# Optimization experiments

Hardware: AMD Instinct MI355X
Metric: run time of the kernel (lower is better)

Reference implementation:

```python
import jax, jax.numpy as jnp
import numpy as np

N, E, G = 40000, 640000, 64
D, H, O = 128, 128, 10
EPS = 1e-5


def _lin(k, fan_in, shape):
    b = 1.0 / np.sqrt(fan_in)
    return jax.random.uniform(k, shape, jnp.float32, -b, b)


def setup_inputs() -> dict:
    key = jax.random.key(0)
    ks = jax.random.split(key, 12)
    x = jax.random.normal(ks[0], (N, D), jnp.float32)
    edge_index = jax.random.randint(ks[1], (2, E), 0, N)
    batch = jnp.sort(jax.random.randint(ks[2], (N,), 0, G))
    return {
        "x": x,
        "edge_index": edge_index,
        "batch": batch,
        "num_graphs": G,
        "W_gcn": _lin(ks[3], D, (D, H)),
        "b_gcn": jnp.zeros((H,), jnp.float32),
        "gamma": jnp.ones((H,), jnp.float32),
        "beta": jnp.zeros((H,), jnp.float32),
        "W1": _lin(ks[4], 3 * H, (3 * H, H)),
        "b1": _lin(ks[5], 3 * H, (H,)),
        "W2": _lin(ks[6], H, (H, H // 2)),
        "b2": _lin(ks[7], H, (H // 2,)),
        "W3": _lin(ks[8], H // 2, (H // 2, O)),
        "b3": _lin(ks[9], H // 2, (O,)),
    }


def reference(x, edge_index, batch, num_graphs, W_gcn, b_gcn, gamma, beta, W1, b1, W2, b2, W3, b3):
    n = x.shape[0]
    src, dst = edge_index[0], edge_index[1]
    # GCNConv: h = D^{-1/2} (A + I) D^{-1/2} (x W) + b  (self-loops, symmetric norm)
    h = x @ W_gcn                                   # [N, H]
    deg = jax.ops.segment_sum(jnp.ones((src.shape[0],), h.dtype), dst, num_segments=n) + 1.0
    dinv = jax.lax.rsqrt(deg)                       # [N]
    coef = dinv[src] * dinv[dst]                    # [E]
    msg = h[src] * coef[:, None]                    # [E, H] gather (memory bound)
    agg = jax.ops.segment_sum(msg, dst, num_segments=n)
    agg = agg + h * (dinv * dinv)[:, None] + b_gcn  # self-loop term + bias
    h = jax.nn.relu(agg)
    # LayerNorm over feature dim
    mu = jnp.mean(h, axis=-1, keepdims=True)
    var = jnp.mean(jnp.square(h - mu), axis=-1, keepdims=True)
    h = (h - mu) * jax.lax.rsqrt(var + EPS) * gamma + beta
    # global mean / add / max pools keyed by graph id
    counts = jax.ops.segment_sum(jnp.ones((n,), h.dtype), batch, num_segments=num_graphs)
    x_add = jax.ops.segment_sum(h, batch, num_segments=num_graphs)
    x_mean = x_add / jnp.maximum(counts, 1.0)[:, None]
    x_max = jax.ops.segment_max(h, batch, num_segments=num_graphs)
    x_max = jnp.where(counts[:, None] > 0, x_max, 0.0)
    g = jnp.concatenate([x_mean, x_add, x_max], axis=1)  # [G, 3H]
    # MLP head (dropout is identity at inference)
    g = jax.nn.relu(g @ W1 + b1)
    g = jax.nn.relu(g @ W2 + b2)
    return g @ W3 + b3
```

## Files before the change

### kernel.cpp

```cpp
#include <hip/hip_runtime.h>
#include <math.h>

#define EPS 1e-5f
#define FLT_BIG 3.402823466e38f

typedef __attribute__((ext_vector_type(8))) short bf16x8;
typedef __attribute__((ext_vector_type(4))) float f32x4;

__device__ __forceinline__ unsigned fflip(float f){
  int i = __float_as_int(f);
  return (unsigned)(i ^ ((i>>31) | 0x80000000));
}
__device__ __forceinline__ float funflip(unsigned u){
  int i = (u & 0x80000000u) ? (int)(u ^ 0x80000000u) : (int)(~u);
  return __int_as_float(i);
}
__device__ __forceinline__ unsigned f2bf(float f){
  unsigned u = __float_as_uint(f);
  return (u + 0x7FFFu + ((u>>16)&1u)) >> 16;
}
__device__ __forceinline__ float bf_lo(unsigned v){ return __uint_as_float(v<<16); }
__device__ __forceinline__ float bf_hi(unsigned v){ return __uint_as_float(v & 0xFFFF0000u); }

__device__ __forceinline__ int lbound(const int* __restrict__ a, int n, int key){
  int lo=0, hi=n;
  while(lo<hi){ int mid=(lo+hi)>>1; if(a[mid]<key) lo=mid+1; else hi=mid; }
  return lo;
}

__global__ __launch_bounds__(256) void k_bucketize(
    const int* __restrict__ src, const int* __restrict__ dst, int E, int NB,
    unsigned* __restrict__ gcur, unsigned* __restrict__ dstream,
    const float* __restrict__ Wg, ushort* __restrict__ Wp,
    const int* __restrict__ batch, int N, int* __restrict__ gcnt, int G){
  __shared__ unsigned hist[160];
  __shared__ unsigned excl[160];
  __shared__ unsigned base[160];
  __shared__ unsigned wsum[4];
  __shared__ unsigned lsorted[2048];
  int t = threadIdx.x, bid = blockIdx.x;

  if(bid < 8){
    int i = bid*256 + t;
    int tile = i>>6, l = i&63;
    int kt = tile>>3, ct = tile&7;
    int q = l>>4, nn = l&15;
    ushort w8[8];
    #pragma unroll
    for(int j=0;j<8;j++)
      w8[j] = (ushort)f2bf(Wg[(kt*32 + q*8 + j)*128 + ct*16 + nn]);
    ushort* dstp = Wp + (size_t)i*8;
    #pragma unroll
    for(int j=0;j<8;j++) dstp[j] = w8[j];
  } else if(bid == 8){
    if(t < G){
      int s = lbound(batch,N,t), e = lbound(batch,N,t+1);
      gcnt[t] = e - s;
    }
  }

  int e0 = bid*2048 + t*8;
  unsigned rec[8]; int bk[8]; unsigned rr[8];
  #pragma unroll
  for(int j=0;j<8;j++) bk[j] = -1;
  if(e0+7 < E){
    int4 s0 = *(const int4*)(src+e0), s1 = *(const int4*)(src+e0+4);
    int4 d0 = *(const int4*)(dst+e0), d1 = *(const int4*)(dst+e0+4);
    int ss[8] = {s0.x,s0.y,s0.z,s0.w,s1.x,s1.y,s1.z,s1.w};
    int dd[8] = {d0.x,d0.y,d0.z,d0.w,d1.x,d1.y,d1.z,d1.w};
    #pragma unroll
    for(int j=0;j<8;j++){
      bk[j] = dd[j]>>8;
      rec[j] = ((unsigned)bk[j]<<24) | ((unsigned)(dd[j]&255)<<16) | (unsigned)ss[j];
    }
  } else {
    #pragma unroll
    for(int j=0;j<8;j++){
      int ee = e0+j;
      if(ee<E){
        int s = src[ee], d = dst[ee];
        bk[j] = d>>8;
        rec[j] = ((unsigned)bk[j]<<24) | ((unsigned)(d&255)<<16) | (unsigned)s;
      }
    }
  }
  for(int i=t;i<NB;i+=256) hist[i]=0u;
  __syncthreads();
  #pragma unroll
  for(int j=0;j<8;j++)
    if(bk[j]>=0) rr[j] = atomicAdd(&hist[bk[j]],1u);
  __syncthreads();
  unsigned hv = (t<NB)?hist[t]:0u;
  unsigned v = hv;
  int lane = t & 63;
  #pragma unroll
  for(int d=1; d<64; d<<=1){
    unsigned o = __shfl_up(v, d, 64);
    if(lane >= d) v += o;
  }
  if(lane==63) wsum[t>>6] = v;
  __syncthreads();
  {
    unsigned pre = 0;
    int w = t>>6;
    if(w>0) pre += wsum[0];
    if(w>1) pre += wsum[1];
    if(w>2) pre += wsum[2];
    if(t<NB) excl[t] = v + pre - hv;
  }
  if(t<NB){
    int ridx = t + bid; while(ridx>=NB) ridx-=NB;
    base[ridx] = atomicAdd(&gcur[ridx], hist[ridx]);
  }
  __syncthreads();
  #pragma unroll
  for(int j=0;j<8;j++)
    if(bk[j]>=0) lsorted[excl[bk[j]]+rr[j]] = rec[j];
  __syncthreads();
  int vc = E - bid*2048; if(vc>2048) vc=2048;
  #pragma unroll
  for(int j=0;j<8;j++){
    int k = j*256 + t;
    if(k<vc){
      unsigned rc = lsorted[k];
      unsigned bb = rc>>24;
      unsigned pos = base[bb] + (unsigned)k - excl[bb];
      if(pos < 8192u) dstream[((size_t)bb<<13) + pos] = rc;
    }
  }
}

__global__ __launch_bounds__(1024) void k_csrscale(
    const unsigned* __restrict__ dstream, const unsigned* __restrict__ gcur,
    int N, ushort* __restrict__ csr, int* __restrict__ cursor,
    const float4* __restrict__ x4, uint2* __restrict__ xs2){
  __shared__ unsigned cnt[256];
  __shared__ float dv[256];
  __shared__ ushort slab[16384];
  int b = blockIdx.x, t = threadIdx.x;
  if(t<256) cnt[t]=0u;
  __syncthreads();
  int nb = (int)gcur[b]; if(nb>8192) nb=8192;
  const unsigned* sp = dstream + ((size_t)b<<13);
  for(int i=t;i<nb;i+=1024){
    unsigned rc = sp[i];
    int dl = (rc>>16)&255;
    unsigned p = atomicAdd(&cnt[dl],1u);
    if(p<64u) slab[(dl<<6)+(int)p] = (ushort)(rc & 0xFFFFu);
  }
  __syncthreads();
  const uint4* s4 = (const uint4*)slab;
  uint4* c4 = ((uint4*)csr) + ((size_t)b<<11);
  #pragma unroll
  for(int i=t;i<2048;i+=1024) c4[i] = s4[i];
  if(t<256){
    int node = (b<<8) + t;
    if(node<N) cursor[node] = (int)cnt[t];
    int deg = (int)cnt[t]; if(deg>64) deg=64;
    dv[t] = rsqrtf((float)deg + 1.0f);
  }
  __syncthreads();
  int base = b<<8;
  for(int i=t; i<8192; i+=1024){
    int nl = i>>5;
    int node = base + nl;
    if(node<N){
      float dinv = dv[nl];
      size_t idx = ((size_t)node<<5) + (i&31);
      float4 v = x4[idx];
      uint2 o;
      o.x = (f2bf(v.y*dinv)<<16) | f2bf(v.x*dinv);
      o.y = (f2bf(v.w*dinv)<<16) | f2bf(v.z*dinv);
      xs2[idx] = o;
    }
  }
}

__global__ void k_agg(const uint4* __restrict__ xs4, const int* __restrict__ cursor,
                      const ushort* __restrict__ csr, int n, uint4* __restrict__ zb4){
  int w = (blockIdx.x*blockDim.x + threadIdx.x)>>6;
  if(w>=n) return;
  int lane = threadIdx.x & 63;
  int grp = lane>>4, li = lane&15;
  int deg = cursor[w]; if(deg>64) deg=64;
  int k0 = w<<6, k1 = k0+deg;
  float dd = rsqrtf((float)deg + 1.0f);
  float a0=0.f,a1=0.f,a2=0.f,a3=0.f,a4=0.f,a5=0.f,a6=0.f,a7=0.f;
  if(grp==0){
    uint4 sv = xs4[(w<<4)+li];
    a0=bf_lo(sv.x); a1=bf_hi(sv.x); a2=bf_lo(sv.y); a3=bf_hi(sv.y);
    a4=bf_lo(sv.z); a5=bf_hi(sv.z); a6=bf_lo(sv.w); a7=bf_hi(sv.w);
  }
  for(int kb=k0; kb<k1; kb+=16){
    int base = kb + (grp<<2);
    ushort4 s4 = *(const ushort4*)(csr + base);
    if(base   < k1){ uint4 v = xs4[((int)s4.x<<4)+li];
      a0+=bf_lo(v.x); a1+=bf_hi(v.x); a2+=bf_lo(v.y); a3+=bf_hi(v.y);
      a4+=bf_lo(v.z); a5+=bf_hi(v.z); a6+=bf_lo(v.w); a7+=bf_hi(v.w); }
    if(base+1 < k1){ uint4 v = xs4[((int)s4.y<<4)+li];
      a0+=bf_lo(v.x); a1+=bf_hi(v.x); a2+=bf_lo(v.y); a3+=bf_hi(v.y);
      a4+=bf_lo(v.z); a5+=bf_hi(v.z); a6+=bf_lo(v.w); a7+=bf_hi(v.w); }
    if(base+2 < k1){ uint4 v = xs4[((int)s4.z<<4)+li];
      a0+=bf_lo(v.x); a1+=bf_hi(v.x); a2+=bf_lo(v.y); a3+=bf_hi(v.y);
      a4+=bf_lo(v.z); a5+=bf_hi(v.z); a6+=bf_lo(v.w); a7+=bf_hi(v.w); }
    if(base+3 < k1){ uint4 v = xs4[((int)s4.w<<4)+li];
      a0+=bf_lo(v.x); a1+=bf_hi(v.x); a2+=bf_lo(v.y); a3+=bf_hi(v.y);
      a4+=bf_lo(v.z); a5+=bf_hi(v.z); a6+=bf_lo(v.w); a7+=bf_hi(v.w); }
  }
  a0 += __shfl_xor(a0,16,64); a1 += __shfl_xor(a1,16,64);
  a2 += __shfl_xor(a2,16,64); a3 += __shfl_xor(a3,16,64);
  a4 += __shfl_xor(a4,16,64); a5 += __shfl_xor(a5,16,64);
  a6 += __shfl_xor(a6,16,64); a7 += __shfl_xor(a7,16,64);
  a0 += __shfl_xor(a0,32,64); a1 += __shfl_xor(a1,32,64);
  a2 += __shfl_xor(a2,32,64); a3 += __shfl_xor(a3,32,64);
  a4 += __shfl_xor(a4,32,64); a5 += __shfl_xor(a5,32,64);
  a6 += __shfl_xor(a6,32,64); a7 += __shfl_xor(a7,32,64);
  if(grp==0){
    uint4 o;
    o.x = (f2bf(a1*dd)<<16) | f2bf(a0*dd);
    o.y = (f2bf(a3*dd)<<16) | f2bf(a2*dd);
    o.z = (f2bf(a5*dd)<<16) | f2bf(a4*dd);
    o.w = (f2bf(a7*dd)<<16) | f2bf(a6*dd);
    zb4[(w<<4)+li] = o;
  }
}

__global__ __launch_bounds__(256) void k_gemmln(
    const unsigned* __restrict__ zb, const ushort* __restrict__ Wp,
    const float* __restrict__ bgc, const float* __restrict__ gamma, const float* __restrict__ beta,
    const int* __restrict__ batch, int n,
    float* __restrict__ pool_sum, unsigned* __restrict__ pool_maxu){
  __shared__ float sred[4][128];
  __shared__ float mred[4][128];
  int t = threadIdx.x, lane = t & 63, wv = t >> 6;
  int rowBase = blockIdx.x*64;
  int q = lane>>4, nn = lane&15;
  int m = rowBase + wv*16 + nn;
  bf16x8 afr[4];
  if(m < n){
    const char* rp = (const char*)zb + (size_t)m*256;
    #pragma unroll
    for(int kt=0;kt<4;kt++)
      afr[kt] = *(const bf16x8*)(rp + kt*64 + q*16);
  } else {
    #pragma unroll
    for(int kt=0;kt<4;kt++) afr[kt] = (bf16x8){0,0,0,0,0,0,0,0};
  }

  f32x4 acc[8];
  #pragma unroll
  for(int ct=0;ct<8;ct++){
    f32x4 c = {0.f,0.f,0.f,0.f};
    #pragma unroll
    for(int kt=0;kt<4;kt++){
      bf16x8 bfr = *(const bf16x8*)(Wp + ((size_t)(kt*8+ct)*64 + lane)*8);
      c = __builtin_amdgcn_mfma_f32_16x16x32_bf16(afr[kt], bfr, c, 0, 0, 0);
    }
    acc[ct] = c;
  }
  float s[4]={0,0,0,0}, qq[4]={0,0,0,0};
  #pragma unroll
  for(int ct=0;ct<8;ct++){
    float bb = bgc[ct*16+nn];
    #pragma unroll
    for(int r=0;r<4;r++){
      float v = acc[ct][r] + bb;
      v = fmaxf(v, 0.f);
      acc[ct][r] = v;
      s[r] += v; qq[r] += v*v;
    }
  }
  #pragma unroll
  for(int d=1; d<16; d<<=1){
    #pragma unroll
    for(int r=0;r<4;r++){
      s[r]  += __shfl_xor(s[r],  d, 64);
      qq[r] += __shfl_xor(qq[r], d, 64);
    }
  }
  float mu[4], isd[4];
  #pragma unroll
  for(int r=0;r<4;r++){
    mu[r] = s[r]*(1.f/128.f);
    float var = qq[r]*(1.f/128.f) - mu[r]*mu[r];
    isd[r] = rsqrtf(var + EPS);
  }
  #pragma unroll
  for(int ct=0;ct<8;ct++){
    float gm = gamma[ct*16+nn], bt = beta[ct*16+nn];
    #pragma unroll
    for(int r=0;r<4;r++)
      acc[ct][r] = (acc[ct][r]-mu[r])*isd[r]*gm + bt;
  }
  int gbr[4];
  #pragma unroll
  for(int r=0;r<4;r++){
    int gr = rowBase + wv*16 + q*4 + r;
    gbr[r] = (gr < n) ? batch[gr] : -1;
  }
  int b0i = rowBase; if(b0i >= n) b0i = n-1;
  int b63i = rowBase + 63; if(b63i >= n) b63i = n-1;
  int gmin = batch[b0i], gmax = batch[b63i];
  if(gmax < gmin) gmax = gmin;
  for(int g=gmin; g<=gmax; ++g){
    #pragma unroll
    for(int ct=0;ct<8;ct++){
      float ssum = 0.f, smax = -FLT_BIG;
      #pragma unroll
      for(int r=0;r<4;r++){
        if(gbr[r]==g){
          ssum += acc[ct][r];
          smax = fmaxf(smax, acc[ct][r]);
        }
      }
      ssum += __shfl_xor(ssum, 16, 64);
      ssum += __shfl_xor(ssum, 32, 64);
      float o1 = __shfl_xor(smax, 16, 64); smax = fmaxf(smax, o1);
      float o2 = __shfl_xor(smax, 32, 64); smax = fmaxf(smax, o2);
      if(q==0){
        sred[wv][ct*16+nn] = ssum;
        mred[wv][ct*16+nn] = smax;
      }
    }
    __syncthreads();
    if(t < 128){
      float s0 = (sred[0][t]+sred[1][t]) + (sred[2][t]+sred[3][t]);
      float m0 = fmaxf(fmaxf(mred[0][t],mred[1][t]), fmaxf(mred[2][t],mred[3][t]));
      if(s0 != 0.f)    atomicAdd(&pool_sum[g*128 + t], s0);
      if(m0 > -FLT_BIG) atomicMax(&pool_maxu[g*128 + t], fflip(m0));
    }
    __syncthreads();
  }
}

__global__ __launch_bounds__(512) void k_head(
    const float* __restrict__ pool_sum, const unsigned* __restrict__ pool_maxu,
    const int* __restrict__ gcnt,
    const float* __restrict__ W1, const float* __restrict__ b1,
    const float* __restrict__ W2, const float* __restrict__ b2,
    const float* __restrict__ W3, const float* __restrict__ b3,
    float* __restrict__ out){
  int g = blockIdx.x, t = threadIdx.x;
  __shared__ float red[4][128];
  __shared__ float gl[384];
  __shared__ float h1[128];
  __shared__ float h2[64];
  int cnt = gcnt[g];
  if(t<384){
    int j = t & 127;
    if(t<128){
      gl[t] = pool_sum[g*128+j] / (float)((cnt>1)?cnt:1);
    } else if(t<256){
      gl[t] = pool_sum[g*128+j];
    } else {
      float m = funflip(pool_maxu[g*128+j]);
      gl[t] = (cnt>0) ? m : 0.f;
    }
  }
  __syncthreads();
  int j = t & 127, kh = t >> 7;
  float p=0.f;
  for(int k=kh*96; k<kh*96+96; k++) p += gl[k]*W1[k*128+j];
  red[kh][j]=p;
  __syncthreads();
  if(t<128){
    float v = red[0][t]+red[1][t]+red[2][t]+red[3][t]+b1[t];
    h1[t]=fmaxf(v,0.f);
  }
  __syncthreads();
  if(t<64){
    float a=b2[t];
    for(int k=0;k<128;k++) a += h1[k]*W2[k*64+t];
    h2[t]=fmaxf(a,0.f);
  }
  __syncthreads();
  if(t<10){
    float a=b3[t];
    for(int k=0;k<64;k++) a += h2[k]*W3[k*10+t];
    out[g*10+t]=a;
  }
}

extern "C" void kernel_launch(void* const* d_in, const int* in_sizes, int n_in,
                              void* d_out, int out_size, void* d_ws, size_t ws_size,
                              hipStream_t stream){
  const float* x     = (const float*)d_in[0];
  const int*   ei    = (const int*)d_in[1];
  const int*   batch = (const int*)d_in[2];
  const float* Wg    = (const float*)d_in[4];
  const float* bg    = (const float*)d_in[5];
  const float* gamma = (const float*)d_in[6];
  const float* beta  = (const float*)d_in[7];
  const float* W1    = (const float*)d_in[8];
  const float* b1    = (const float*)d_in[9];
  const float* W2    = (const float*)d_in[10];
  const float* b2    = (const float*)d_in[11];
  const float* W3    = (const float*)d_in[12];
  const float* b3    = (const float*)d_in[13];
  float* out = (float*)d_out;

  int N = in_sizes[0]/128;
  int E = in_sizes[1]/2;
  const int G = 64;
  const int* src = ei;
  const int* dst = ei + E;
  int NB = (N+255)>>8;

  char* p = (char*)d_ws;
  auto alloc=[&](size_t bytes)->char*{ char* r=p; p += (bytes+255)&~(size_t)255; return r; };
  size_t zr_bytes = (size_t)G*128*4 + (size_t)G*128*4 + 1024;
  char*     zr      = alloc(zr_bytes);
  float*    psum    = (float*)zr;
  unsigned* pmaxu   = (unsigned*)(zr + (size_t)G*128*4);
  unsigned* gcur    = (unsigned*)(zr + (size_t)G*128*4*2);
  int*      cursor  = (int*)     alloc((size_t)N*4);
  ushort*   csr     = (ushort*)  alloc((size_t)NB*16384*2);
  unsigned* zb      = (unsigned*)alloc((size_t)N*64*4);
  unsigned* xs      = (unsigned*)alloc((size_t)N*64*4);
  ushort*   Wp      = (ushort*)  alloc(2048*8*2);
  int*      gcnt    = (int*)     alloc((size_t)G*4);
  unsigned* dstream = (unsigned*)alloc((size_t)NB*8192*4);

  hipMemsetAsync(zr, 0, zr_bytes, stream);
  int bb = (E+2047)/2048;
  k_bucketize<<<bb,256,0,stream>>>(src,dst,E,NB,gcur,dstream,Wg,Wp,batch,N,gcnt,G);
  k_csrscale<<<NB,1024,0,stream>>>(dstream,gcur,N,csr,cursor,(const float4*)x,(uint2*)xs);
  int ab = (int)(((size_t)N*64 + 255)/256);
  k_agg<<<ab,256,0,stream>>>((const uint4*)xs,cursor,csr,N,(uint4*)zb);
  k_gemmln<<<(N+63)/64,256,0,stream>>>(zb,Wp,bg,gamma,beta,batch,N,psum,pmaxu);
  k_head<<<G,512,0,stream>>>(psum,pmaxu,gcnt,W1,b1,W2,b2,W3,b3,out);
}
```

Measured before the change: 161.2 us.

## Pad CSR with zero-row sentinel and split bucketize histogram per wave

The bucketize kernel now keeps a separate LDS histogram for each wave and combines them with per-wave prefix offsets, which cuts contention on shared-memory atomics. The CSR slab is pre-filled with index N, which points at an added all-zero row of xs. The aggregation loop can then drop its per-neighbor bounds checks and always issue four gathers per group. The cost is extra gathers of the zero row for padding slots, plus extra LDS initialisation and an extra row of workspace.

```diff
diff --git a/kernel.cpp b/kernel.cpp
--- a/kernel.cpp
+++ b/kernel.cpp
@@ -33,12 +33,14 @@
     unsigned* __restrict__ gcur, unsigned* __restrict__ dstream,
     const float* __restrict__ Wg, ushort* __restrict__ Wp,
     const int* __restrict__ batch, int N, int* __restrict__ gcnt, int G){
+  __shared__ unsigned whist[4][160];
   __shared__ unsigned hist[160];
   __shared__ unsigned excl[160];
   __shared__ unsigned base[160];
   __shared__ unsigned wsum[4];
   __shared__ unsigned lsorted[2048];
   int t = threadIdx.x, bid = blockIdx.x;
+  int wid = t>>6, lane = t&63;
 
   if(bid < 8){
     int i = bid*256 + t;
@@ -84,28 +86,34 @@
       }
     }
   }
-  for(int i=t;i<NB;i+=256) hist[i]=0u;
+  for(int i=t;i<NB;i+=256){
+    whist[0][i]=0u; whist[1][i]=0u; whist[2][i]=0u; whist[3][i]=0u;
+  }
   __syncthreads();
   #pragma unroll
   for(int j=0;j<8;j++)
-    if(bk[j]>=0) rr[j] = atomicAdd(&hist[bk[j]],1u);
-  __syncthreads();
-  unsigned hv = (t<NB)?hist[t]:0u;
+    if(bk[j]>=0) rr[j] = atomicAdd(&whist[wid][bk[j]],1u);
+  __syncthreads();
+  unsigned hv = 0u;
+  if(t<NB){
+    unsigned h0=whist[0][t], h1=whist[1][t], h2=whist[2][t], h3=whist[3][t];
+    hv = h0+h1+h2+h3;
+    hist[t] = hv;
+    whist[0][t]=0u; whist[1][t]=h0; whist[2][t]=h0+h1; whist[3][t]=h0+h1+h2;
+  }
   unsigned v = hv;
-  int lane = t & 63;
   #pragma unroll
   for(int d=1; d<64; d<<=1){
     unsigned o = __shfl_up(v, d, 64);
     if(lane >= d) v += o;
   }
-  if(lane==63) wsum[t>>6] = v;
+  if(lane==63) wsum[wid] = v;
   __syncthreads();
   {
     unsigned pre = 0;
-    int w = t>>6;
-    if(w>0) pre += wsum[0];
-    if(w>1) pre += wsum[1];
-    if(w>2) pre += wsum[2];
+    if(wid>0) pre += wsum[0];
+    if(wid>1) pre += wsum[1];
+    if(wid>2) pre += wsum[2];
     if(t<NB) excl[t] = v + pre - hv;
   }
   if(t<NB){
@@ -115,7 +123,7 @@
   __syncthreads();
   #pragma unroll
   for(int j=0;j<8;j++)
-    if(bk[j]>=0) lsorted[excl[bk[j]]+rr[j]] = rec[j];
+    if(bk[j]>=0) lsorted[excl[bk[j]] + whist[wid][bk[j]] + rr[j]] = rec[j];
   __syncthreads();
   int vc = E - bid*2048; if(vc>2048) vc=2048;
   #pragma unroll
@@ -139,6 +147,13 @@
   __shared__ ushort slab[16384];
   int b = blockIdx.x, t = threadIdx.x;
   if(t<256) cnt[t]=0u;
+  {
+    unsigned sv = ((unsigned)N<<16) | (unsigned)N;
+    uint4 fillv = make_uint4(sv,sv,sv,sv);
+    #pragma unroll
+    for(int i=t;i<2048;i+=1024) ((uint4*)slab)[i] = fillv;
+  }
+  if(b==0 && t<16) ((uint4*)(xs2 + ((size_t)N<<5)))[t] = make_uint4(0,0,0,0);
   __syncthreads();
   int nb = (int)gcur[b]; if(nb>8192) nb=8192;
   const unsigned* sp = dstream + ((size_t)b<<13);
@@ -183,7 +198,7 @@
   int lane = threadIdx.x & 63;
   int grp = lane>>4, li = lane&15;
   int deg = cursor[w]; if(deg>64) deg=64;
-  int k0 = w<<6, k1 = k0+deg;
+  int k0 = w<<6;
   float dd = rsqrtf((float)deg + 1.0f);
   float a0=0.f,a1=0.f,a2=0.f,a3=0.f,a4=0.f,a5=0.f,a6=0.f,a7=0.f;
   if(grp==0){
@@ -191,19 +206,19 @@
     a0=bf_lo(sv.x); a1=bf_hi(sv.x); a2=bf_lo(sv.y); a3=bf_hi(sv.y);
     a4=bf_lo(sv.z); a5=bf_hi(sv.z); a6=bf_lo(sv.w); a7=bf_hi(sv.w);
   }
-  for(int kb=k0; kb<k1; kb+=16){
-    int base = kb + (grp<<2);
+  for(int kb=0; kb<deg; kb+=16){
+    int base = k0 + kb + (grp<<2);
     ushort4 s4 = *(const ushort4*)(csr + base);
-    if(base   < k1){ uint4 v = xs4[((int)s4.x<<4)+li];
+    { uint4 v = xs4[((int)s4.x<<4)+li];
       a0+=bf_lo(v.x); a1+=bf_hi(v.x); a2+=bf_lo(v.y); a3+=bf_hi(v.y);
       a4+=bf_lo(v.z); a5+=bf_hi(v.z); a6+=bf_lo(v.w); a7+=bf_hi(v.w); }
-    if(base+1 < k1){ uint4 v = xs4[((int)s4.y<<4)+li];
+    { uint4 v = xs4[((int)s4.y<<4)+li];
       a0+=bf_lo(v.x); a1+=bf_hi(v.x); a2+=bf_lo(v.y); a3+=bf_hi(v.y);
       a4+=bf_lo(v.z); a5+=bf_hi(v.z); a6+=bf_lo(v.w); a7+=bf_hi(v.w); }
-    if(base+2 < k1){ uint4 v = xs4[((int)s4.z<<4)+li];
+    { uint4 v = xs4[((int)s4.z<<4)+li];
       a0+=bf_lo(v.x); a1+=bf_hi(v.x); a2+=bf_lo(v.y); a3+=bf_hi(v.y);
       a4+=bf_lo(v.z); a5+=bf_hi(v.z); a6+=bf_lo(v.w); a7+=bf_hi(v.w); }
-    if(base+3 < k1){ uint4 v = xs4[((int)s4.w<<4)+li];
+    { uint4 v = xs4[((int)s4.w<<4)+li];
       a0+=bf_lo(v.x); a1+=bf_hi(v.x); a2+=bf_lo(v.y); a3+=bf_hi(v.y);
       a4+=bf_lo(v.z); a5+=bf_hi(v.z); a6+=bf_lo(v.w); a7+=bf_hi(v.w); }
   }
@@ -416,7 +431,7 @@
   int*      cursor  = (int*)     alloc((size_t)N*4);
   ushort*   csr     = (ushort*)  alloc((size_t)NB*16384*2);
   unsigned* zb      = (unsigned*)alloc((size_t)N*64*4);
-  unsigned* xs      = (unsigned*)alloc((size_t)N*64*4);
+  unsigned* xs      = (unsigned*)alloc((size_t)(N+1)*64*4);
   ushort*   Wp      = (ushort*)  alloc(2048*8*2);
   int*      gcnt    = (int*)     alloc((size_t)G*4);
   unsigned* dstream = (unsigned*)alloc((size_t)NB*8192*4);
```

Result: faster. 156.8 us, median of 2 (-2.7%).
